# Kernel tuning notes

Measured on AMD Instinct MI355X. Metric: run time of the kernel, lower is better.

Reference implementation:

```python
import jax, jax.numpy as jnp
import numpy as np

B, N, M12, H, O, I, DIFF = 8192, 100, 12, 64, 128, 12, 1.0
TWO_PI = 2.0 * np.pi


def _moments_single(xi, K):
    # xi: [N, 2] single sample; K: [12, 2] exponent pairs -> [12]
    xc = xi - xi.mean(axis=0)                 # center per-sample (mean over points)
    p = xc[:, None, :] ** K[None, :, :]       # [N, 12, 2]
    return jnp.sum(p[..., 0] * p[..., 1], axis=0)  # [12]


def setup_inputs() -> dict:
    key = jax.random.key(0)
    ks = jax.random.split(key, 8)
    # 12 integer central-moment exponent pairs (p, q)
    P = jnp.array([1, 2, 0, 2, 1, 3, 0, 2, 3, 1, 4, 0], jnp.float32)
    Q = jnp.array([1, 0, 2, 1, 2, 0, 3, 2, 1, 3, 0, 4], jnp.float32)
    K = jnp.stack([P, Q], axis=-1)            # [12, 2]

    x = jax.random.normal(ks[0], (B, N, 2), jnp.float32)
    t = jax.random.uniform(ks[1], (1,), jnp.float32, 0.1, 1.0)  # positive time
    W_fourier = jax.random.normal(ks[2], (H // 2,), jnp.float32) * 30.0

    def lin(k, fin, fout):
        bound = 1.0 / np.sqrt(fin)
        kw, kb = jax.random.split(k)
        W = jax.random.uniform(kw, (fin, fout), jnp.float32, -bound, bound)
        b = jax.random.uniform(kb, (fout,), jnp.float32, -bound, bound)
        return W, b

    embed_W, embed_b = lin(ks[3], H, H)
    lin1_W, lin1_b = lin(ks[4], I, H)
    lin2a_W, lin2a_b = lin(ks[5], H, O)
    lin2b_W, lin2b_b = lin(ks[6], O, I)
    lin2c_W, lin2c_b = lin(ks[7], I, I)
    return {
        'x': x, 't': t, 'K': K, 'W_fourier': W_fourier,
        'embed_W': embed_W, 'embed_b': embed_b,
        'lin1_W': lin1_W, 'lin1_b': lin1_b,
        'lin2a_W': lin2a_W, 'lin2a_b': lin2a_b,
        'lin2b_W': lin2b_W, 'lin2b_b': lin2b_b,
        'lin2c_W': lin2c_W, 'lin2c_b': lin2c_b,
    }


def reference(x, t, K, W_fourier, embed_W, embed_b, lin1_W, lin1_b,
              lin2a_W, lin2a_b, lin2b_W, lin2b_b, lin2c_W, lin2c_b):
    # Invariance encoding ('Moment' mode): [B, 12]
    m = jax.vmap(_moments_single, in_axes=(0, None))(x, K)
    h = jax.nn.gelu(m @ lin1_W + lin1_b, approximate=False)   # [B, H] (dropout = eval identity)
    # Gaussian Fourier time embedding: [1, H]
    xp = t[:, None] * W_fourier[None, :] * TWO_PI
    emb = jnp.concatenate([jnp.sin(xp), jnp.cos(xp)], axis=-1) @ embed_W + embed_b
    h = jax.nn.gelu((h + emb) @ lin2a_W + lin2a_b, approximate=False)
    h = jax.nn.gelu(h @ lin2b_W + lin2b_b, approximate=False)
    h = (h @ lin2c_W + lin2c_b) / jnp.sqrt(DIFF * t)          # [B, 12]
    # Per-sample jacobian of the moment map: [B, 12, N, 2]
    # (equals the block diagonal of torch.autograd.functional.jacobian over the batch)
    jac = jax.vmap(jax.jacrev(_moments_single), in_axes=(0, None))(x, K)
    # Replaces the (i, j) double loop of tiny matmuls with one batched contraction
    return jnp.einsum('bk,bknj->bnj', h, jac)                 # [B, N, 2]
```

## Files before the change

kernel.cpp:

```cpp
#include <hip/hip_runtime.h>


static __device__ __forceinline__ float gelu_f(float x) {
    float y = 0.7071067811865475f * x;
    float s = fabsf(y);
    float t = __builtin_amdgcn_rcpf(fmaf(0.3275911f, s, 1.0f));
    float p = t * fmaf(t, fmaf(t, fmaf(t, fmaf(t, 1.061405429f,
                    -1.453152027f), 1.421413741f), -0.284496736f), 0.254829592f);
    float e = __expf(-y * y);
    float ea = fmaf(-p, e, 1.0f);
    float erfv = copysignf(ea, y);
    return 0.5f * x * (1.0f + erfv);
}

#define DPP_ADD(v, ctrl) \
    v += __int_as_float(__builtin_amdgcn_update_dpp(0, __float_as_int(v), ctrl, 0xf, 0xf, true))

static __device__ __forceinline__ float wave_sum(float v) {
    DPP_ADD(v, 0x111);
    DPP_ADD(v, 0x112);
    DPP_ADD(v, 0x114);
    DPP_ADD(v, 0x118);
    DPP_ADD(v, 0x142);
    DPP_ADD(v, 0x143);
    return __int_as_float(__builtin_amdgcn_readlane(__float_as_int(v), 63));
}

#define TWO_PI_F 6.283185307179586f

__global__ __launch_bounds__(256) void scorenet_fused(
    const float* __restrict__ x,
    const float* __restrict__ t_in,
    const float* __restrict__ Wf,
    const float* __restrict__ embW,
    const float* __restrict__ embB,
    const float* __restrict__ W1,
    const float* __restrict__ b1,
    const float* __restrict__ W2a,
    const float* __restrict__ b2a,
    const float* __restrict__ W2b,
    const float* __restrict__ b2b,
    const float* __restrict__ W2c,
    const float* __restrict__ b2c,
    float* __restrict__ out,
    int B)
{
    __shared__ float s_f[64];
    __shared__ float s_emb[64];
    __shared__ float s_a[64][4];
    __shared__ float s_part[4][2][4][64];

    const int tid = threadIdx.x;
    const int lane = tid & 63;
    const int w = tid >> 6;
    const float tval = t_in[0];

    const int b = blockIdx.x * 4 + w;
    const bool valid = b < B;
    const int bc = valid ? b : B - 1;

    const float2* px = reinterpret_cast<const float2*>(x) + (size_t)bc * 100;
    const bool has2 = lane < 36;
    float2 p0 = px[lane];
    float2 p1 = px[has2 ? lane + 64 : lane];

    if (tid < 32) {
        float xp = tval * Wf[tid] * TWO_PI_F;
        s_f[tid]      = sinf(xp);
        s_f[tid + 32] = cosf(xp);
    }
    __syncthreads();
    if (tid < 64) {
        float acc = embB[tid];
        const float4* f4 = reinterpret_cast<const float4*>(s_f);
        #pragma unroll
        for (int c = 0; c < 16; ++c) {
            float4 a4 = f4[c];
            int j = 4 * c;
            acc = fmaf(a4.x, embW[(j+0)*64 + tid],
                  fmaf(a4.y, embW[(j+1)*64 + tid],
                  fmaf(a4.z, embW[(j+2)*64 + tid],
                  fmaf(a4.w, embW[(j+3)*64 + tid], acc))));
        }
        s_emb[tid] = acc;
    }
    __syncthreads();

    float xa = p0.x, ya = p0.y;
    float xb = has2 ? p1.x : 0.0f;
    float yb = has2 ? p1.y : 0.0f;

    const float mux = wave_sum(xa + xb) * 0.01f;
    const float muy = wave_sum(ya + yb) * 0.01f;

    float ua = xa - mux, va = ya - muy;
    float ub = has2 ? (xb - mux) : 0.0f;
    float vb = has2 ? (yb - muy) : 0.0f;

    float ms[12];
    {
        float u2 = ua * ua, v2 = va * va;
        ms[0] = ua * va;   ms[1] = u2;        ms[2] = v2;
        ms[3] = u2 * va;   ms[4] = ua * v2;
        ms[5] = u2 * ua;   ms[6] = v2 * va;
        ms[7] = u2 * v2;   ms[8] = ms[5] * va; ms[9] = ua * ms[6];
        ms[10] = u2 * u2;  ms[11] = v2 * v2;
        float w2 = ub * ub, z2 = vb * vb;
        ms[0] += ub * vb;  ms[1] += w2;       ms[2] += z2;
        ms[3] += w2 * vb;  ms[4] += ub * z2;
        ms[5] += w2 * ub;  ms[6] += z2 * vb;
        ms[7] += w2 * z2;  ms[8] += w2 * ub * vb; ms[9] += ub * z2 * vb;
        ms[10] += w2 * w2; ms[11] += z2 * z2;
    }
    float m[12];
    #pragma unroll
    for (int k = 0; k < 12; ++k) m[k] = wave_sum(ms[k]);

    float a1 = b1[lane];
    #pragma unroll
    for (int k = 0; k < 12; ++k) a1 = fmaf(m[k], W1[k * 64 + lane], a1);
    float aval = gelu_f(a1) + s_emb[lane];

    s_a[lane][w] = aval;
    __syncthreads();

    float4 plo = {0.f, 0.f, 0.f, 0.f};
    float4 phi = {0.f, 0.f, 0.f, 0.f};
    {
        const float4* a4p = reinterpret_cast<const float4*>(&s_a[0][0]);
        const float2* w2a2 = reinterpret_cast<const float2*>(W2a);
        #pragma unroll
        for (int jj = 0; jj < 16; ++jj) {
            const int j = (w << 4) + jj;
            float4 a4 = a4p[j];
            float2 ww = w2a2[j * 64 + lane];
            plo.x = fmaf(a4.x, ww.x, plo.x);
            plo.y = fmaf(a4.y, ww.x, plo.y);
            plo.z = fmaf(a4.z, ww.x, plo.z);
            plo.w = fmaf(a4.w, ww.x, plo.w);
            phi.x = fmaf(a4.x, ww.y, phi.x);
            phi.y = fmaf(a4.y, ww.y, phi.y);
            phi.z = fmaf(a4.z, ww.y, phi.z);
            phi.w = fmaf(a4.w, ww.y, phi.w);
        }
    }
    s_part[0][0][w][lane] = plo.x;
    s_part[1][0][w][lane] = plo.y;
    s_part[2][0][w][lane] = plo.z;
    s_part[3][0][w][lane] = plo.w;
    s_part[0][1][w][lane] = phi.x;
    s_part[1][1][w][lane] = phi.y;
    s_part[2][1][w][lane] = phi.z;
    s_part[3][1][w][lane] = phi.w;
    __syncthreads();

    const float2 bb2a = reinterpret_cast<const float2*>(b2a)[lane];
    float acc0 = bb2a.x + ((s_part[w][0][0][lane] + s_part[w][0][1][lane])
                         + (s_part[w][0][2][lane] + s_part[w][0][3][lane]));
    float acc1 = bb2a.y + ((s_part[w][1][0][lane] + s_part[w][1][1][lane])
                         + (s_part[w][1][2][lane] + s_part[w][1][3][lane]));
    float h2lo = gelu_f(acc0), h2hi = gelu_f(acc1);

    const float4* w2b4 = reinterpret_cast<const float4*>(W2b);
    float4 l0 = w2b4[lane * 6 + 0], l1 = w2b4[lane * 6 + 1], l2 = w2b4[lane * 6 + 2];
    float4 u0 = w2b4[lane * 6 + 3], u1 = w2b4[lane * 6 + 4], u2 = w2b4[lane * 6 + 5];
    const float wl[12] = {l0.x,l0.y,l0.z,l0.w, l1.x,l1.y,l1.z,l1.w, l2.x,l2.y,l2.z,l2.w};
    const float wu[12] = {u0.x,u0.y,u0.z,u0.w, u1.x,u1.y,u1.z,u1.w, u2.x,u2.y,u2.z,u2.w};
    float h3[12];
    #pragma unroll
    for (int k = 0; k < 12; ++k) {
        float p3 = fmaf(h2lo, wl[k], h2hi * wu[k]);
        h3[k] = gelu_f(wave_sum(p3) + b2b[k]);
    }

    const float rst = rsqrtf(tval);
    float hk = 0.0f;
    if (lane < 12) {
        hk = b2c[lane];
        #pragma unroll
        for (int j = 0; j < 12; ++j) hk = fmaf(h3[j], W2c[j * 12 + lane], hk);
        hk *= rst;
    }
    float h[12];
    #pragma unroll
    for (int k = 0; k < 12; ++k)
        h[k] = __int_as_float(__builtin_amdgcn_readlane(__float_as_int(hk), k));

    const float inv_n = 0.01f;
    float c0 = (2.0f*h[3]*m[0] + h[4]*m[2] + 3.0f*h[5]*m[1] + 2.0f*h[7]*m[4]
              + 3.0f*h[8]*m[3] + h[9]*m[6] + 4.0f*h[10]*m[5]) * inv_n;
    float c1 = (h[3]*m[1] + 2.0f*h[4]*m[0] + 3.0f*h[6]*m[2] + 2.0f*h[7]*m[3]
              + h[8]*m[5] + 3.0f*h[9]*m[4] + 4.0f*h[11]*m[6]) * inv_n;

    const float A1 = 2.0f*h[1], A2 = h[0],      A3 = 3.0f*h[5], A4 = 2.0f*h[3], A5 = h[4];
    const float A6 = 4.0f*h[10],A7 = 3.0f*h[8], A8 = 2.0f*h[7], A9 = h[9];
    const float B1 = h[0],      B2 = 2.0f*h[2], B3 = h[3],      B4 = 2.0f*h[4], B5 = 3.0f*h[6];
    const float B6 = h[8],      B7 = 2.0f*h[7], B8 = 3.0f*h[9], B9 = 4.0f*h[11];

    float2* pout = reinterpret_cast<float2*>(out) + (size_t)bc * 100;
    if (valid) {
        float u = ua, v = va;
        float u2 = u*u, v2 = v*v;
        float o0 = A1*u + A2*v + A3*u2 + A4*u*v + A5*v2 + A6*u2*u + A7*u2*v + A8*u*v2 + A9*v2*v - c0;
        float o1 = B1*u + B2*v + B3*u2 + B4*u*v + B5*v2 + B6*u2*u + B7*u2*v + B8*u*v2 + B9*v2*v - c1;
        float2 r; r.x = o0; r.y = o1;
        pout[lane] = r;
        if (has2) {
            float uu = ub, vv = vb;
            float uu2 = uu*uu, vv2 = vv*vv;
            float q0 = A1*uu + A2*vv + A3*uu2 + A4*uu*vv + A5*vv2 + A6*uu2*uu + A7*uu2*vv + A8*uu*vv2 + A9*vv2*vv - c0;
            float q1 = B1*uu + B2*vv + B3*uu2 + B4*uu*vv + B5*vv2 + B6*uu2*uu + B7*uu2*vv + B8*uu*vv2 + B9*vv2*vv - c1;
            float2 r2; r2.x = q0; r2.y = q1;
            pout[lane + 64] = r2;
        }
    }
}

extern "C" void kernel_launch(void* const* d_in, const int* in_sizes, int n_in,
                              void* d_out, int out_size, void* d_ws, size_t ws_size,
                              hipStream_t stream) {
    const float* x    = (const float*)d_in[0];
    const float* t    = (const float*)d_in[1];
    const float* Wf   = (const float*)d_in[3];
    const float* embW = (const float*)d_in[4];
    const float* embB = (const float*)d_in[5];
    const float* W1   = (const float*)d_in[6];
    const float* b1   = (const float*)d_in[7];
    const float* W2a  = (const float*)d_in[8];
    const float* b2a  = (const float*)d_in[9];
    const float* W2b  = (const float*)d_in[10];
    const float* b2b  = (const float*)d_in[11];
    const float* W2c  = (const float*)d_in[12];
    const float* b2c  = (const float*)d_in[13];

    const int B = in_sizes[0] / 200;
    const int blocks = (B + 3) / 4;

    scorenet_fused<<<blocks, 256, 0, stream>>>(
        x, t, Wf, embW, embB, W1, b1, W2a, b2a, W2b, b2b, W2c, b2c,
        (float*)d_out, B);
}
```

Baseline: 96.53 us.

## Precompute time embedding in separate kernel and stage W2b transposed in LDS

The Fourier time embedding (sin/cos plus a 64x64 matvec) and rsqrt(t) move into a tiny one-block kernel that writes them to workspace. The main kernel reads these from global memory, so it no longer repeats that work in every block or waits on two block barriers for it. The main kernel also stages W2b transposed into shared memory so each lane reads a contiguous float2 per output column instead of strided float4 global loads. The trade-offs are an extra kernel launch with a dependency between the two kernels, and transposed LDS writes that may hit bank conflicts.

```diff
diff --git a/kernel.cpp b/kernel.cpp
--- a/kernel.cpp
+++ b/kernel.cpp
@@ -28,12 +28,40 @@
 
 #define TWO_PI_F 6.283185307179586f
 
-__global__ __launch_bounds__(256) void scorenet_fused(
-    const float* __restrict__ x,
+__global__ __launch_bounds__(64) void emb_precompute(
     const float* __restrict__ t_in,
     const float* __restrict__ Wf,
     const float* __restrict__ embW,
     const float* __restrict__ embB,
+    float* __restrict__ ws)
+{
+    __shared__ float s_f[64];
+    const int tid = threadIdx.x;
+    const float tval = t_in[0];
+    if (tid < 32) {
+        float xp = tval * Wf[tid] * TWO_PI_F;
+        s_f[tid]      = sinf(xp);
+        s_f[tid + 32] = cosf(xp);
+    }
+    __syncthreads();
+    float acc = embB[tid];
+    const float4* f4 = reinterpret_cast<const float4*>(s_f);
+    #pragma unroll
+    for (int c = 0; c < 16; ++c) {
+        float4 a4 = f4[c];
+        int j = 4 * c;
+        acc = fmaf(a4.x, embW[(j+0)*64 + tid],
+              fmaf(a4.y, embW[(j+1)*64 + tid],
+              fmaf(a4.z, embW[(j+2)*64 + tid],
+              fmaf(a4.w, embW[(j+3)*64 + tid], acc))));
+    }
+    ws[tid] = acc;
+    if (tid == 0) ws[64] = rsqrtf(tval);
+}
+
+__global__ __launch_bounds__(256) void scorenet_fused(
+    const float* __restrict__ x,
+    const float* __restrict__ emb_ws,
     const float* __restrict__ W1,
     const float* __restrict__ b1,
     const float* __restrict__ W2a,
@@ -45,15 +73,13 @@
     float* __restrict__ out,
     int B)
 {
-    __shared__ float s_f[64];
-    __shared__ float s_emb[64];
     __shared__ float s_a[64][4];
     __shared__ float s_part[4][2][4][64];
+    __shared__ float s_w2bT[12][128];
 
     const int tid = threadIdx.x;
     const int lane = tid & 63;
     const int w = tid >> 6;
-    const float tval = t_in[0];
 
     const int b = blockIdx.x * 4 + w;
     const bool valid = b < B;
@@ -64,27 +90,14 @@
     float2 p0 = px[lane];
     float2 p1 = px[has2 ? lane + 64 : lane];
 
-    if (tid < 32) {
-        float xp = tval * Wf[tid] * TWO_PI_F;
-        s_f[tid]      = sinf(xp);
-        s_f[tid + 32] = cosf(xp);
-    }
-    __syncthreads();
-    if (tid < 64) {
-        float acc = embB[tid];
-        const float4* f4 = reinterpret_cast<const float4*>(s_f);
-        #pragma unroll
-        for (int c = 0; c < 16; ++c) {
-            float4 a4 = f4[c];
-            int j = 4 * c;
-            acc = fmaf(a4.x, embW[(j+0)*64 + tid],
-                  fmaf(a4.y, embW[(j+1)*64 + tid],
-                  fmaf(a4.z, embW[(j+2)*64 + tid],
-                  fmaf(a4.w, embW[(j+3)*64 + tid], acc))));
-        }
-        s_emb[tid] = acc;
-    }
-    __syncthreads();
+    #pragma unroll
+    for (int i = tid; i < 1536; i += 256) {
+        int row = i / 12, col = i - row * 12;
+        s_w2bT[col][row] = W2b[i];
+    }
+
+    const float emb_lane = emb_ws[lane];
+    const float rst = emb_ws[64];
 
     float xa = p0.x, ya = p0.y;
     float xb = has2 ? p1.x : 0.0f;
@@ -119,7 +132,7 @@
     float a1 = b1[lane];
     #pragma unroll
     for (int k = 0; k < 12; ++k) a1 = fmaf(m[k], W1[k * 64 + lane], a1);
-    float aval = gelu_f(a1) + s_emb[lane];
+    float aval = gelu_f(a1) + emb_lane;
 
     s_a[lane][w] = aval;
     __syncthreads();
@@ -161,19 +174,14 @@
                          + (s_part[w][1][2][lane] + s_part[w][1][3][lane]));
     float h2lo = gelu_f(acc0), h2hi = gelu_f(acc1);
 
-    const float4* w2b4 = reinterpret_cast<const float4*>(W2b);
-    float4 l0 = w2b4[lane * 6 + 0], l1 = w2b4[lane * 6 + 1], l2 = w2b4[lane * 6 + 2];
-    float4 u0 = w2b4[lane * 6 + 3], u1 = w2b4[lane * 6 + 4], u2 = w2b4[lane * 6 + 5];
-    const float wl[12] = {l0.x,l0.y,l0.z,l0.w, l1.x,l1.y,l1.z,l1.w, l2.x,l2.y,l2.z,l2.w};
-    const float wu[12] = {u0.x,u0.y,u0.z,u0.w, u1.x,u1.y,u1.z,u1.w, u2.x,u2.y,u2.z,u2.w};
     float h3[12];
     #pragma unroll
     for (int k = 0; k < 12; ++k) {
-        float p3 = fmaf(h2lo, wl[k], h2hi * wu[k]);
+        float2 wk = *reinterpret_cast<const float2*>(&s_w2bT[k][2 * lane]);
+        float p3 = fmaf(h2lo, wk.x, h2hi * wk.y);
         h3[k] = gelu_f(wave_sum(p3) + b2b[k]);
     }
 
-    const float rst = rsqrtf(tval);
     float hk = 0.0f;
     if (lane < 12) {
         hk = b2c[lane];
@@ -235,8 +243,10 @@
 
     const int B = in_sizes[0] / 200;
     const int blocks = (B + 3) / 4;
-
+    float* ws = (float*)d_ws;
+
+    emb_precompute<<<1, 64, 0, stream>>>(t, Wf, embW, embB, ws);
     scorenet_fused<<<blocks, 256, 0, stream>>>(
-        x, t, Wf, embW, embB, W1, b1, W2a, b2a, W2b, b2b, W2c, b2c,
+        x, ws, W1, b1, W2a, b2a, W2b, b2b, W2c, b2c,
         (float*)d_out, B);
 }
```

After: 99.08 us. 1.03x slower.
